# Kernel tuning notes

Hardware: AMD Instinct MI355X
Metric: run time of the kernel (lower is better)

## Reference

```python
import jax, jax.numpy as jnp
import numpy as np

B, C_IN, T, N = 16, 64, 12, 1024
KS, C_OUT = 3, 64


def setup_inputs() -> dict:
    key = jax.random.key(0)
    k1, k2, k3 = jax.random.split(key, 3)
    x = jax.random.normal(k1, (B, C_IN, T, N), dtype=jnp.float32)
    # graph Chebyshev kernel [N, Ks*N]; scale down so matmuls stay well-conditioned
    kernel = jax.random.normal(k2, (N, KS * N), dtype=jnp.float32) / np.sqrt(N)
    # xavier-uniform theta [Ks*c_in, c_out]
    limit = np.sqrt(6.0 / (KS * C_IN + C_OUT))
    theta = jax.random.uniform(k3, (KS * C_IN, C_OUT), dtype=jnp.float32,
                               minval=-limit, maxval=limit)
    bias = jnp.zeros((C_OUT,), dtype=jnp.float32)
    return {"x": x, "kernel": kernel, "theta": theta, "bias": bias}


def reference(x, kernel, theta, bias):
    # x: [B, C, T, N]; kernel: [N, Ks*N] viewed as [N, Ks, N]; theta: [C*Ks, c_out]
    Bb, C, Tt, Nn = x.shape
    Ks = kernel.shape[1] // Nn
    Kr = kernel.reshape(Nn, Ks, Nn)            # [n, k, m]
    th = theta.reshape(C, Ks, -1)              # [c, k, o] (row index = c*Ks + k)
    # batched spectral conv over all timesteps at once (fuses the per-t loop)
    x_mul = jnp.einsum('bctn,nkm->bctkm', x, Kr)       # [B,C,T,Ks,N]
    gc = jnp.einsum('bctkm,cko->botm', x_mul, th)      # [B,c_out,T,N]
    gc = gc + bias[None, :, None, None]
    # c_in == c_out -> residual is identity
    return jax.nn.relu(gc + x)
```

## Files before the change

kernel.cpp:

```cpp
#include <hip/hip_runtime.h>

#define NB   16
#define NC   64
#define NT   12
#define NN   1024
#define NKS  3

typedef float  f32x4  __attribute__((ext_vector_type(4)));
typedef short  s16x8  __attribute__((ext_vector_type(8)));
typedef unsigned short u16x4 __attribute__((ext_vector_type(4)));
typedef unsigned short u16x8 __attribute__((ext_vector_type(8)));
typedef unsigned short ush;

__device__ __forceinline__ ush f2bf(float f) {
    union { float f; unsigned u; } v; v.f = f;
    unsigned r = v.u + 0x7FFFu + ((v.u >> 16) & 1u);
    return (ush)(r >> 16);
}
__device__ __forceinline__ float bf2f(ush h) {
    union { unsigned u; float f; } v; v.u = ((unsigned)h) << 16;
    return v.f;
}

__device__ __forceinline__ void cp16(const void* g, void* l) {
    __builtin_amdgcn_global_load_lds(
        (const __attribute__((address_space(1))) unsigned int*)g,
        (__attribute__((address_space(3))) unsigned int*)l, 16, 0, 0);
}

#define APAN_OFF 0
#define KB_OFF   25165824
#define TH_OFF   31457280

__global__ __launch_bounds__(256)
void spatio_prep(const float* __restrict__ x, const float* __restrict__ kern,
                 const float* __restrict__ theta,
                 ush* __restrict__ apan, ush* __restrict__ kb, ush* __restrict__ thbf)
{
    const int blk = blockIdx.x;
    const int tid = threadIdx.x;

    if (blk < 1536) {
        int ch   = blk * 256 + tid;
        int p    = ch & 3;
        int j    = (ch >> 2) % 192;
        int rest = (ch >> 2) / 192;
        int nb   = rest & 31, mt = rest >> 5;
        int d    = p ^ (j & 3);
        int k    = j >> 6, mm = j & 63;
        int col  = (k << 10) + (mt << 6) + mm;
        u16x8 w;
#pragma unroll
        for (int i = 0; i < 8; ++i) {
            int n = nb * 32 + d * 8 + i;
            w[i] = f2bf(kern[(size_t)n * (NKS * NN) + col]);
        }
        ((u16x8*)kb)[ch] = w;
    } else if (blk < 1584) {
        int id = (blk - 1536) * 256 + tid;
        if (id < 12288) {
            int row = id >> 6, o = id & 63;
            int c = row / 3, k = row - 3 * c;
            thbf[o * 192 + k * 64 + c] = f2bf(theta[id]);
        }
    } else {
        int id   = (blk - 1584) * 256 + tid;
        int slot = id & 511;
        int g2nb = id >> 9;
        int nb   = g2nb & 31, g2 = g2nb >> 5;
        int row  = slot >> 2, p = slot & 3;
        int d    = p ^ (row & 3);
        int bl   = row >> 6, c = row & 63;
        int bt   = 2 * g2 + bl;
        int b    = bt / NT, t = bt - NT * b;
        const float* src = x + ((size_t)((b * NC + c) * NT + t)) * NN + nb * 32 + d * 8;
        float4 a0 = ((const float4*)src)[0];
        float4 a1 = ((const float4*)src)[1];
        u16x8 w;
        w[0] = f2bf(a0.x); w[1] = f2bf(a0.y); w[2] = f2bf(a0.z); w[3] = f2bf(a0.w);
        w[4] = f2bf(a1.x); w[5] = f2bf(a1.y); w[6] = f2bf(a1.z); w[7] = f2bf(a1.w);
        ((u16x8*)apan)[id] = w;
    }
}

__global__ __launch_bounds__(256, 2)
void spatio_main(const ush* __restrict__ apan, const ush* __restrict__ kb,
                 const ush* __restrict__ thbf, const float* __restrict__ bias,
                 float* __restrict__ out)
{
    __shared__ __attribute__((aligned(128))) char smem[57344];
    ush (*xm)[200] = (ush (*)[200])smem;
    ush (*stL)[32] = (ush (*)[32])(smem + 40960);
    ush (*stH)[32] = (ush (*)[32])(smem + 49152);

    const int tid  = threadIdx.x;
    const int g2   = blockIdx.x;
    const int mt   = blockIdx.y;
    const int m_base = mt * 64;
    const int lane = tid & 63;
    const int wid  = tid >> 6;
    const int wr   = wid & 1;
    const int wn   = wid >> 1;
    const int quad = lane >> 4;
    const int l16  = lane & 15;
    const int pofs = (quad ^ (l16 & 3)) * 8;

    const char* apan_c = (const char*)apan + ((size_t)g2 << 18);
    const char* kb_c   = (const char*)kb + ((size_t)mt * 32 * 768 * 16);

    f32x4 acc[4][6];
#pragma unroll
    for (int i = 0; i < 4; ++i)
#pragma unroll
        for (int j = 0; j < 6; ++j) acc[i][j] = (f32x4){0.f, 0.f, 0.f, 0.f};

#pragma unroll
    for (int i = 0; i < 2; ++i)
        cp16(apan_c + (i * 256 + tid) * 16, smem + (i * 256 + tid) * 16);
#pragma unroll
    for (int i = 0; i < 3; ++i)
        cp16(kb_c + (i * 256 + tid) * 16, smem + 8192 + (i * 256 + tid) * 16);

    for (int it = 0; it < 32; ++it) {
        const int p = it & 1;
        char* buf = smem + p * 20480;
        __syncthreads();
        if (it < 31) {
            const char* asrc = apan_c + ((size_t)(it + 1) << 13);
            const char* bsrc = kb_c + (size_t)(it + 1) * 12288;
            char* nbuf = smem + (p ^ 1) * 20480;
#pragma unroll
            for (int i = 0; i < 2; ++i)
                cp16(asrc + (i * 256 + tid) * 16, nbuf + (i * 256 + tid) * 16);
#pragma unroll
            for (int i = 0; i < 3; ++i)
                cp16(bsrc + (i * 256 + tid) * 16, nbuf + 8192 + (i * 256 + tid) * 16);
        }
        if ((it >> 1) == mt) {
            const char* asrc = apan_c + ((size_t)it << 13);
            char* sb = smem + 40960 + (it & 1) * 8192;
#pragma unroll
            for (int i = 0; i < 2; ++i) {
                int m = i * 256 + tid;
                int slot = (m & ~3) + ((m & 3) ^ ((m >> 2) & 3));
                cp16(asrc + slot * 16, sb + m * 16);
            }
        }

        ush (*As)[32] = (ush (*)[32])buf;
        ush (*Bs)[32] = (ush (*)[32])(buf + 8192);
        s16x8 af[4], bf[6];
#pragma unroll
        for (int rb = 0; rb < 4; ++rb)
            af[rb] = *(const s16x8*)&As[64 * wr + 16 * rb + l16][pofs];
#pragma unroll
        for (int jb = 0; jb < 6; ++jb)
            bf[jb] = *(const s16x8*)&Bs[96 * wn + 16 * jb + l16][pofs];
#pragma unroll
        for (int rb = 0; rb < 4; ++rb)
#pragma unroll
            for (int jb = 0; jb < 6; ++jb)
                acc[rb][jb] = __builtin_amdgcn_mfma_f32_16x16x32_bf16(af[rb], bf[jb], acc[rb][jb], 0, 0, 0);
    }

    float bo[4];
#pragma unroll
    for (int r = 0; r < 4; ++r) bo[r] = bias[16 * wid + 4 * quad + r];

    for (int pass = 0; pass < 2; ++pass) {
        __syncthreads();
        if (wr == pass) {
#pragma unroll
            for (int rb = 0; rb < 4; ++rb)
#pragma unroll
                for (int jb = 0; jb < 6; ++jb) {
                    int J  = 96 * wn + 16 * jb + l16;
                    int kk = J >> 6, mm = J & 63;
                    int ck0 = kk * 64 + 16 * rb + 4 * quad;
                    u16x4 w;
                    w.x = f2bf(acc[rb][jb].x); w.y = f2bf(acc[rb][jb].y);
                    w.z = f2bf(acc[rb][jb].z); w.w = f2bf(acc[rb][jb].w);
                    *(u16x4*)&xm[mm][ck0] = w;
                }
        }
        __syncthreads();

        f32x4 acc2[4];
#pragma unroll
        for (int jb = 0; jb < 4; ++jb) acc2[jb] = (f32x4){0.f, 0.f, 0.f, 0.f};
#pragma unroll
        for (int ks = 0; ks < 6; ++ks) {
            s16x8 a2 = *(const s16x8*)(thbf + (size_t)(16 * wid + l16) * 192 + ks * 32 + quad * 8);
#pragma unroll
            for (int jb = 0; jb < 4; ++jb) {
                s16x8 b2 = *(const s16x8*)&xm[16 * jb + l16][ks * 32 + quad * 8];
                acc2[jb] = __builtin_amdgcn_mfma_f32_16x16x32_bf16(a2, b2, acc2[jb], 0, 0, 0);
            }
        }

        const int bt = 2 * g2 + pass;
        const int b2i = bt / NT, t2 = bt - NT * b2i;
#pragma unroll
        for (int jb = 0; jb < 4; ++jb) {
            int mm = 16 * jb + l16;
#pragma unroll
            for (int r = 0; r < 4; ++r) {
                int o = 16 * wid + 4 * quad + r;
                int row = pass * 64 + o;
                ush rv = (jb < 2) ? stL[row][mm] : stH[row][mm - 32];
                size_t idx = (((size_t)(b2i * NC + o) * NT + t2) * NN) + m_base + mm;
                float v = acc2[jb][r] + bo[r] + bf2f(rv);
                out[idx] = fmaxf(v, 0.f);
            }
        }
    }
}

extern "C" void kernel_launch(void* const* d_in, const int* in_sizes, int n_in,
                              void* d_out, int out_size, void* d_ws, size_t ws_size,
                              hipStream_t stream) {
    const float* x     = (const float*)d_in[0];
    const float* kern  = (const float*)d_in[1];
    const float* theta = (const float*)d_in[2];
    const float* bias  = (const float*)d_in[3];
    float* out = (float*)d_out;
    (void)in_sizes; (void)n_in; (void)out_size; (void)ws_size;

    ush* apan = (ush*)((char*)d_ws + APAN_OFF);
    ush* kbp  = (ush*)((char*)d_ws + KB_OFF);
    ush* thbf = (ush*)((char*)d_ws + TH_OFF);

    hipLaunchKernelGGL(spatio_prep, dim3(7728), dim3(256), 0, stream,
                       x, kern, theta, apan, kbp, thbf);
    hipLaunchKernelGGL(spatio_main, dim3(96, 16), dim3(256), 0, stream,
                       apan, kbp, thbf, bias, out);
}
```

Baseline: 186.3 us.

## Double the main-kernel row tile to four timesteps with 512-thread blocks

The main GEMM block now covers four (b,t) slices instead of two, using 8 waves and a larger shared-memory double buffer, so each kernel-matrix tile loaded from global memory is reused across twice as many rows. The prep kernel is reorganized to match the new 256-row panel layout and has each thread convert two 16-byte chunks. The aim is to halve the global traffic for the large Chebyshev kernel operand. The cost is much more LDS per block (about 88 KB), which may lower occupancy, and the epilogue now runs four serialized passes.

```diff
diff --git a/kernel.cpp b/kernel.cpp
--- a/kernel.cpp
+++ b/kernel.cpp
@@ -65,48 +65,56 @@
         }
     } else {
         int id   = (blk - 1584) * 256 + tid;
-        int slot = id & 511;
-        int g2nb = id >> 9;
-        int nb   = g2nb & 31, g2 = g2nb >> 5;
-        int row  = slot >> 2, p = slot & 3;
-        int d    = p ^ (row & 3);
+        int ch0  = id * 2;
+        int slot = ch0 & 1023;
+        int g4nb = ch0 >> 10;
+        int nb   = g4nb & 31, g4 = g4nb >> 5;
+        int row  = slot >> 2;
+        int q2   = slot & 3;
+        int d0   = q2 ^ (row & 3);
+        int dbase = d0 & ~1;
         int bl   = row >> 6, c = row & 63;
-        int bt   = 2 * g2 + bl;
+        int bt   = 4 * g4 + bl;
         int b    = bt / NT, t = bt - NT * b;
-        const float* src = x + ((size_t)((b * NC + c) * NT + t)) * NN + nb * 32 + d * 8;
-        float4 a0 = ((const float4*)src)[0];
-        float4 a1 = ((const float4*)src)[1];
-        u16x8 w;
-        w[0] = f2bf(a0.x); w[1] = f2bf(a0.y); w[2] = f2bf(a0.z); w[3] = f2bf(a0.w);
-        w[4] = f2bf(a1.x); w[5] = f2bf(a1.y); w[6] = f2bf(a1.z); w[7] = f2bf(a1.w);
-        ((u16x8*)apan)[id] = w;
+        const float* src = x + ((size_t)((b * NC + c) * NT + t)) * NN + nb * 32 + dbase * 8;
+        float4 v0 = ((const float4*)src)[0];
+        float4 v1 = ((const float4*)src)[1];
+        float4 v2 = ((const float4*)src)[2];
+        float4 v3 = ((const float4*)src)[3];
+        u16x8 lo, hi;
+        lo[0]=f2bf(v0.x); lo[1]=f2bf(v0.y); lo[2]=f2bf(v0.z); lo[3]=f2bf(v0.w);
+        lo[4]=f2bf(v1.x); lo[5]=f2bf(v1.y); lo[6]=f2bf(v1.z); lo[7]=f2bf(v1.w);
+        hi[0]=f2bf(v2.x); hi[1]=f2bf(v2.y); hi[2]=f2bf(v2.z); hi[3]=f2bf(v2.w);
+        hi[4]=f2bf(v3.x); hi[5]=f2bf(v3.y); hi[6]=f2bf(v3.z); hi[7]=f2bf(v3.w);
+        ((u16x8*)apan)[ch0]     = (d0 & 1) ? hi : lo;
+        ((u16x8*)apan)[ch0 + 1] = (d0 & 1) ? lo : hi;
     }
 }
 
-__global__ __launch_bounds__(256, 2)
+__global__ __launch_bounds__(512, 2)
 void spatio_main(const ush* __restrict__ apan, const ush* __restrict__ kb,
                  const ush* __restrict__ thbf, const float* __restrict__ bias,
                  float* __restrict__ out)
 {
-    __shared__ __attribute__((aligned(128))) char smem[57344];
+    __shared__ __attribute__((aligned(128))) char smem[90112];
     ush (*xm)[200] = (ush (*)[200])smem;
-    ush (*stL)[32] = (ush (*)[32])(smem + 40960);
-    ush (*stH)[32] = (ush (*)[32])(smem + 49152);
+    ush (*stA)[32] = (ush (*)[32])(smem + 57344);
+    ush (*stB)[32] = (ush (*)[32])(smem + 73728);
 
     const int tid  = threadIdx.x;
-    const int g2   = blockIdx.x;
+    const int g4   = blockIdx.x;
     const int mt   = blockIdx.y;
     const int m_base = mt * 64;
     const int lane = tid & 63;
     const int wid  = tid >> 6;
-    const int wr   = wid & 1;
-    const int wn   = wid >> 1;
+    const int wr   = wid >> 1;
+    const int wn   = wid & 1;
     const int quad = lane >> 4;
     const int l16  = lane & 15;
     const int pofs = (quad ^ (l16 & 3)) * 8;
 
-    const char* apan_c = (const char*)apan + ((size_t)g2 << 18);
-    const char* kb_c   = (const char*)kb + ((size_t)mt * 32 * 768 * 16);
+    const char* apan_c = (const char*)apan + ((size_t)g4 << 19);
+    const char* kb_c   = (const char*)kb + ((size_t)mt * 393216);
 
     f32x4 acc[4][6];
 #pragma unroll
@@ -116,39 +124,39 @@
 
 #pragma unroll
     for (int i = 0; i < 2; ++i)
-        cp16(apan_c + (i * 256 + tid) * 16, smem + (i * 256 + tid) * 16);
-#pragma unroll
-    for (int i = 0; i < 3; ++i)
-        cp16(kb_c + (i * 256 + tid) * 16, smem + 8192 + (i * 256 + tid) * 16);
+        cp16(apan_c + (i * 512 + tid) * 16, smem + (i * 512 + tid) * 16);
+    cp16(kb_c + tid * 16, smem + 16384 + tid * 16);
+    if (tid < 256)
+        cp16(kb_c + (512 + tid) * 16, smem + 16384 + (512 + tid) * 16);
 
     for (int it = 0; it < 32; ++it) {
         const int p = it & 1;
-        char* buf = smem + p * 20480;
+        char* buf = smem + p * 28672;
         __syncthreads();
         if (it < 31) {
-            const char* asrc = apan_c + ((size_t)(it + 1) << 13);
+            const char* asrc = apan_c + ((size_t)(it + 1) << 14);
             const char* bsrc = kb_c + (size_t)(it + 1) * 12288;
-            char* nbuf = smem + (p ^ 1) * 20480;
+            char* nbuf = smem + (p ^ 1) * 28672;
 #pragma unroll
             for (int i = 0; i < 2; ++i)
-                cp16(asrc + (i * 256 + tid) * 16, nbuf + (i * 256 + tid) * 16);
-#pragma unroll
-            for (int i = 0; i < 3; ++i)
-                cp16(bsrc + (i * 256 + tid) * 16, nbuf + 8192 + (i * 256 + tid) * 16);
+                cp16(asrc + (i * 512 + tid) * 16, nbuf + (i * 512 + tid) * 16);
+            cp16(bsrc + tid * 16, nbuf + 16384 + tid * 16);
+            if (tid < 256)
+                cp16(bsrc + (512 + tid) * 16, nbuf + 16384 + (512 + tid) * 16);
         }
         if ((it >> 1) == mt) {
-            const char* asrc = apan_c + ((size_t)it << 13);
-            char* sb = smem + 40960 + (it & 1) * 8192;
+            const char* asrc = apan_c + ((size_t)it << 14);
+            char* sb = smem + 57344 + (it & 1) * 16384;
 #pragma unroll
             for (int i = 0; i < 2; ++i) {
-                int m = i * 256 + tid;
-                int slot = (m & ~3) + ((m & 3) ^ ((m >> 2) & 3));
+                int m = i * 512 + tid;
+                int slot = (m & ~3) | ((m & 3) ^ ((m >> 2) & 3));
                 cp16(asrc + slot * 16, sb + m * 16);
             }
         }
 
         ush (*As)[32] = (ush (*)[32])buf;
-        ush (*Bs)[32] = (ush (*)[32])(buf + 8192);
+        ush (*Bs)[32] = (ush (*)[32])(buf + 16384);
         s16x8 af[4], bf[6];
 #pragma unroll
         for (int rb = 0; rb < 4; ++rb)
@@ -163,11 +171,13 @@
                 acc[rb][jb] = __builtin_amdgcn_mfma_f32_16x16x32_bf16(af[rb], bf[jb], acc[rb][jb], 0, 0, 0);
     }
 
+    const int oh2 = wid & 3;
+    const int mh  = wid >> 2;
     float bo[4];
 #pragma unroll
-    for (int r = 0; r < 4; ++r) bo[r] = bias[16 * wid + 4 * quad + r];
-
-    for (int pass = 0; pass < 2; ++pass) {
+    for (int r = 0; r < 4; ++r) bo[r] = bias[16 * oh2 + 4 * quad + r];
+
+    for (int pass = 0; pass < 4; ++pass) {
         __syncthreads();
         if (wr == pass) {
 #pragma unroll
@@ -175,39 +185,39 @@
 #pragma unroll
                 for (int jb = 0; jb < 6; ++jb) {
                     int J  = 96 * wn + 16 * jb + l16;
-                    int kk = J >> 6, mm = J & 63;
+                    int kk = J >> 6, mmw = J & 63;
                     int ck0 = kk * 64 + 16 * rb + 4 * quad;
                     u16x4 w;
                     w.x = f2bf(acc[rb][jb].x); w.y = f2bf(acc[rb][jb].y);
                     w.z = f2bf(acc[rb][jb].z); w.w = f2bf(acc[rb][jb].w);
-                    *(u16x4*)&xm[mm][ck0] = w;
+                    *(u16x4*)&xm[mmw][ck0] = w;
                 }
         }
         __syncthreads();
 
-        f32x4 acc2[4];
-#pragma unroll
-        for (int jb = 0; jb < 4; ++jb) acc2[jb] = (f32x4){0.f, 0.f, 0.f, 0.f};
+        f32x4 acc2[2];
+#pragma unroll
+        for (int jb = 0; jb < 2; ++jb) acc2[jb] = (f32x4){0.f, 0.f, 0.f, 0.f};
 #pragma unroll
         for (int ks = 0; ks < 6; ++ks) {
-            s16x8 a2 = *(const s16x8*)(thbf + (size_t)(16 * wid + l16) * 192 + ks * 32 + quad * 8);
-#pragma unroll
-            for (int jb = 0; jb < 4; ++jb) {
-                s16x8 b2 = *(const s16x8*)&xm[16 * jb + l16][ks * 32 + quad * 8];
+            s16x8 a2 = *(const s16x8*)(thbf + (size_t)(16 * oh2 + l16) * 192 + ks * 32 + quad * 8);
+#pragma unroll
+            for (int jb = 0; jb < 2; ++jb) {
+                s16x8 b2 = *(const s16x8*)&xm[16 * (2 * mh + jb) + l16][ks * 32 + quad * 8];
                 acc2[jb] = __builtin_amdgcn_mfma_f32_16x16x32_bf16(a2, b2, acc2[jb], 0, 0, 0);
             }
         }
 
-        const int bt = 2 * g2 + pass;
+        const int bt = 4 * g4 + pass;
         const int b2i = bt / NT, t2 = bt - NT * b2i;
 #pragma unroll
-        for (int jb = 0; jb < 4; ++jb) {
-            int mm = 16 * jb + l16;
+        for (int jb = 0; jb < 2; ++jb) {
+            int mm = 16 * (2 * mh + jb) + l16;
 #pragma unroll
             for (int r = 0; r < 4; ++r) {
-                int o = 16 * wid + 4 * quad + r;
+                int o = 16 * oh2 + 4 * quad + r;
                 int row = pass * 64 + o;
-                ush rv = (jb < 2) ? stL[row][mm] : stH[row][mm - 32];
+                ush rv = mh ? stB[row][mm - 32] : stA[row][mm];
                 size_t idx = (((size_t)(b2i * NC + o) * NT + t2) * NN) + m_base + mm;
                 float v = acc2[jb][r] + bo[r] + bf2f(rv);
                 out[idx] = fmaxf(v, 0.f);
@@ -230,8 +240,8 @@
     ush* kbp  = (ush*)((char*)d_ws + KB_OFF);
     ush* thbf = (ush*)((char*)d_ws + TH_OFF);
 
-    hipLaunchKernelGGL(spatio_prep, dim3(7728), dim3(256), 0, stream,
+    hipLaunchKernelGGL(spatio_prep, dim3(4656), dim3(256), 0, stream,
                        x, kern, theta, apan, kbp, thbf);
-    hipLaunchKernelGGL(spatio_main, dim3(96, 16), dim3(256), 0, stream,
+    hipLaunchKernelGGL(spatio_main, dim3(48, 16), dim3(512), 0, stream,
                        apan, kbp, thbf, bias, out);
 }
```

Measured after the change: 204.3 us. 9.7% more time.
